# Kernel tuning notes

Hardware: AMD Instinct MI355X
Metric: run time of the kernel (lower is better)

Reference implementation:

```python
import jax, jax.numpy as jnp
import numpy as np

N, F, D, H = 8192, 128, 128, 2
LEAKY_ALPHA = 0.3  # keras.layers.LeakyReLU default


def setup_inputs() -> dict:
    key = jax.random.key(0)
    ks = jax.random.split(key, 8)
    x = jax.random.normal(ks[0], (N, F), dtype=jnp.float32)
    # sparse-ish binary adjacency with self loops, stored dense (as the module does)
    adj = (jax.random.uniform(ks[1], (N, N)) < 0.01).astype(jnp.float32)
    adj = jnp.clip(adj + jnp.eye(N, dtype=jnp.float32), 0.0, 1.0)
    s = 1.0 / np.sqrt(F)
    Wmap = jax.random.normal(ks[2], (H, F, D), dtype=jnp.float32) * s
    a1_w = jax.random.normal(ks[3], (H, D), dtype=jnp.float32) * (1.0 / np.sqrt(D))
    a2_w = jax.random.normal(ks[4], (H, D), dtype=jnp.float32) * (1.0 / np.sqrt(D))
    a1_b = jnp.zeros((H,), dtype=jnp.float32)
    a2_b = jnp.zeros((H,), dtype=jnp.float32)
    kernel = jax.random.normal(ks[5], (H, F, D), dtype=jnp.float32) * s
    bias = jnp.zeros((H, N, D), dtype=jnp.float32)
    return {"x": x, "adj": adj, "Wmap": Wmap, "a1_w": a1_w, "a1_b": a1_b,
            "a2_w": a2_w, "a2_b": a2_b, "kernel": kernel, "bias": bias}


def reference(x, adj, Wmap, a1_w, a1_b, a2_w, a2_b, kernel, bias):
    # per-head Conv1D(k=1, no bias): node-wise linear map  [H, N, D]
    mapped = jnp.einsum('nf,hfd->hnd', x, Wmap)
    # per-head Conv1D(k=1) scalar scores  [H, N]
    sa1 = jnp.einsum('hnd,hd->hn', mapped, a1_w) + a1_b[:, None]
    sa2 = jnp.einsum('hnd,hd->hn', mapped, a2_w) + a2_b[:, None]
    # additive score masked multiplicatively by adjacency:  [H, N, N]
    w = adj[None, :, :] * sa1[:, :, None] + adj[None, :, :] * sa2[:, None, :]
    w = jnp.where(w >= 0, w, LEAKY_ALPHA * w)
    att = jax.nn.softmax(w, axis=-1)  # softmax over neighbors (incl. zeroed entries, as in source)
    value = jnp.einsum('nf,hfd->hnd', x, kernel)
    out = jnp.einsum('hnm,hmd->hnd', att, value) + bias  # [H, N, D]
    return out.mean(axis=0)  # attn_heads_reduction='average', linear activation
```

## Files before the change

kernel.cpp:

```cpp
#include <hip/hip_runtime.h>

#define NN 8192
#define FF 128
#define DD 128
#define HH 2
#define ALPHA 0.3f
#define MAXNNZ 1024

typedef float v4f __attribute__((ext_vector_type(4)));

__global__ __launch_bounds__(256) void prep_kernel(
    const float* __restrict__ Wmap, const float* __restrict__ a1w,
    const float* __restrict__ a2w, const float* __restrict__ x,
    float* __restrict__ c1, float* __restrict__ c2, float* __restrict__ xsum) {
  int b = blockIdx.x;
  int t = threadIdx.x;
  if (b == 128) {
    int h = t >> 7, f = t & 127;
    const float* wrow = Wmap + ((size_t)h * FF + f) * DD;
    const float* a1 = a1w + h * DD;
    const float* a2 = a2w + h * DD;
    float s1 = 0.f, s2 = 0.f;
    #pragma unroll 8
    for (int d = 0; d < DD; d++) {
      float w = wrow[d];
      s1 += w * a1[d];
      s2 += w * a2[d];
    }
    c1[t] = s1;
    c2[t] = s2;
  } else {
    int f = t & 127, rh = t >> 7;
    const float* xp = x + ((size_t)(b * 64 + rh) * FF) + f;
    float s = 0.f;
    #pragma unroll 8
    for (int r = 0; r < 64; r += 2) s += xp[(size_t)r * FF];
    atomicAdd(&xsum[f], s);
  }
}

__global__ __launch_bounds__(128) void sa_kernel(
    const float* __restrict__ x, const float* __restrict__ c1,
    const float* __restrict__ c2, const float* __restrict__ a1b,
    const float* __restrict__ a2b, float* __restrict__ sa1, float* __restrict__ sa2p) {
  int n = blockIdx.x;
  int f = threadIdx.x;
  float xv = x[(size_t)n * FF + f];
  float p00 = xv * c1[f];
  float p01 = xv * c1[FF + f];
  float p10 = xv * c2[f];
  float p11 = xv * c2[FF + f];
  #pragma unroll
  for (int o = 32; o > 0; o >>= 1) {
    p00 += __shfl_down(p00, o);
    p01 += __shfl_down(p01, o);
    p10 += __shfl_down(p10, o);
    p11 += __shfl_down(p11, o);
  }
  __shared__ float part[2][4];
  int w = f >> 6;
  if ((f & 63) == 0) {
    part[w][0] = p00; part[w][1] = p01; part[w][2] = p10; part[w][3] = p11;
  }
  __syncthreads();
  if (f == 0) {
    sa1[n]      = part[0][0] + part[1][0] + a1b[0];
    sa1[NN + n] = part[0][1] + part[1][1] + a1b[1];
    ((float2*)sa2p)[n] = make_float2(part[0][2] + part[1][2] + a2b[0],
                                     part[0][3] + part[1][3] + a2b[1]);
  }
}

__global__ __launch_bounds__(256) void adj_scan(
    const float* __restrict__ adj, int* __restrict__ counts,
    int* __restrict__ idxw) {
  int i = blockIdx.x;
  __shared__ int idxbuf[MAXNNZ];
  __shared__ int cnt;
  int t = threadIdx.x;
  if (t == 0) cnt = 0;
  __syncthreads();
  const v4f* arow = (const v4f*)(adj + (size_t)i * NN);
  #pragma unroll
  for (int q = 0; q < 8; q++) {
    int f4 = q * 256 + t;
    v4f a = __builtin_nontemporal_load(&arow[f4]);
    int j0 = f4 * 4;
    if (a.x != 0.f) { int p = atomicAdd(&cnt, 1); if (p < MAXNNZ) idxbuf[p] = j0; }
    if (a.y != 0.f) { int p = atomicAdd(&cnt, 1); if (p < MAXNNZ) idxbuf[p] = j0 + 1; }
    if (a.z != 0.f) { int p = atomicAdd(&cnt, 1); if (p < MAXNNZ) idxbuf[p] = j0 + 2; }
    if (a.w != 0.f) { int p = atomicAdd(&cnt, 1); if (p < MAXNNZ) idxbuf[p] = j0 + 3; }
  }
  __syncthreads();
  int count = min(cnt, MAXNNZ);
  if (t == 0) counts[i] = count;
  int* dst = idxw + (size_t)i * MAXNNZ;
  for (int k = t; k < count; k += 256) dst[k] = idxbuf[k];
}

__global__ __launch_bounds__(256) void edge_gather(
    const int* __restrict__ counts, const int* __restrict__ idxw,
    const float* __restrict__ x, const float* __restrict__ sa1,
    const float* __restrict__ sa2p, const float* __restrict__ xsum,
    float* __restrict__ gs) {
  int i = blockIdx.x;
  __shared__ int idxbuf[MAXNNZ];
  __shared__ float em1buf[HH][MAXNNZ];
  __shared__ float wred[4][HH];
  __shared__ float sume_sh[HH];
  __shared__ v4f vred[HH][8][32];
  int t = threadIdx.x;
  int count = counts[i];
  const int* src = idxw + (size_t)i * MAXNNZ;
  for (int k = t; k < count; k += 256) idxbuf[k] = src[k];
  __syncthreads();

  float s10 = sa1[i];
  float s11 = sa1[NN + i];
  float l0 = 0.f, l1 = 0.f;
  for (int k = t; k < count; k += 256) {
    int j = idxbuf[k];
    float2 s2 = ((const float2*)sa2p)[j];
    float w0 = s10 + s2.x;
    float w1 = s11 + s2.y;
    w0 = (w0 >= 0.f) ? w0 : ALPHA * w0;
    w1 = (w1 >= 0.f) ? w1 : ALPHA * w1;
    float e0 = __expf(w0) - 1.f;
    float e1 = __expf(w1) - 1.f;
    em1buf[0][k] = e0;
    em1buf[1][k] = e1;
    l0 += e0;
    l1 += e1;
  }
  #pragma unroll
  for (int o = 32; o > 0; o >>= 1) {
    l0 += __shfl_down(l0, o);
    l1 += __shfl_down(l1, o);
  }
  int wid = t >> 6;
  if ((t & 63) == 0) { wred[wid][0] = l0; wred[wid][1] = l1; }
  __syncthreads();
  if (t == 0) {
    sume_sh[0] = wred[0][0] + wred[1][0] + wred[2][0] + wred[3][0];
    sume_sh[1] = wred[0][1] + wred[1][1] + wred[2][1] + wred[3][1];
  }
  __syncthreads();

  int sub = t & 31;
  int eg  = t >> 5;
  v4f acc0 = {0.f, 0.f, 0.f, 0.f}, acc1 = {0.f, 0.f, 0.f, 0.f};
  const v4f* xb = (const v4f*)x;
  #pragma unroll 4
  for (int k = eg; k < count; k += 8) {
    int j = idxbuf[k];
    v4f xv = xb[(size_t)j * 32 + sub];
    acc0 += em1buf[0][k] * xv;
    acc1 += em1buf[1][k] * xv;
  }
  vred[0][eg][sub] = acc0;
  vred[1][eg][sub] = acc1;
  __syncthreads();
  if (t < 64) {
    int h = t >> 5, s = t & 31;
    v4f v = vred[h][0][s];
    #pragma unroll
    for (int e = 1; e < 8; e++) v += vred[h][e][s];
    float inv = 0.5f / ((float)NN + sume_sh[h]);
    v4f xs = ((const v4f*)xsum)[s];
    v4f g = (v + xs) * inv;
    ((v4f*)(gs + (size_t)i * (HH * FF)))[h * 32 + s] = g;
  }
}

__global__ __launch_bounds__(256) void out_gemm(
    const float* __restrict__ gs, const float* __restrict__ kern,
    const float* __restrict__ bias, float* __restrict__ out) {
  int row0 = blockIdx.x * 32;
  __shared__ float Bl[64 * 128];
  __shared__ float Al[32 * 132];
  const float4* Bg4 = (const float4*)kern;
  const float4* Ag4 = (const float4*)(gs + (size_t)row0 * 256);
  float4* Bl4 = (float4*)Bl;
  int tid = threadIdx.x;
  int cg = tid & 31;
  int rg = tid >> 5;
  v4f acc[4];
  #pragma unroll
  for (int m = 0; m < 4; m++) acc[m] = (v4f){0.f, 0.f, 0.f, 0.f};

  for (int ka = 0; ka < 2; ka++) {
    __syncthreads();
    #pragma unroll
    for (int q = 0; q < 4; q++) {
      int idx = q * 256 + tid;
      int r = idx >> 5, c4 = idx & 31;
      float4 g = Ag4[r * 64 + ka * 32 + c4];
      *(float4*)&Al[r * 132 + c4 * 4] = g;
    }
    #pragma unroll
    for (int kpi = 0; kpi < 2; kpi++) {
      int kp = ka * 2 + kpi;
      __syncthreads();
      #pragma unroll
      for (int q = 0; q < 8; q++)
        Bl4[q * 256 + tid] = Bg4[kp * 2048 + q * 256 + tid];
      __syncthreads();
      #pragma unroll 4
      for (int kg = 0; kg < 16; kg++) {
        v4f bv0 = *(const v4f*)&Bl[(kg * 4 + 0) * 128 + cg * 4];
        v4f bv1 = *(const v4f*)&Bl[(kg * 4 + 1) * 128 + cg * 4];
        v4f bv2 = *(const v4f*)&Bl[(kg * 4 + 2) * 128 + cg * 4];
        v4f bv3 = *(const v4f*)&Bl[(kg * 4 + 3) * 128 + cg * 4];
        #pragma unroll
        for (int m = 0; m < 4; m++) {
          v4f a4 = *(const v4f*)&Al[(rg + m * 8) * 132 + kpi * 64 + kg * 4];
          acc[m] += a4.x * bv0;
          acc[m] += a4.y * bv1;
          acc[m] += a4.z * bv2;
          acc[m] += a4.w * bv3;
        }
      }
    }
  }

  #pragma unroll
  for (int m = 0; m < 4; m++) {
    int r = row0 + rg + m * 8;
    v4f b0 = *(const v4f*)&bias[((size_t)0 * NN + r) * DD + cg * 4];
    v4f b1 = *(const v4f*)&bias[((size_t)1 * NN + r) * DD + cg * 4];
    v4f o = acc[m] + 0.5f * (b0 + b1);
    *(v4f*)&out[(size_t)r * DD + cg * 4] = o;
  }
}

extern "C" void kernel_launch(void* const* d_in, const int* in_sizes, int n_in,
                              void* d_out, int out_size, void* d_ws, size_t ws_size,
                              hipStream_t stream) {
  const float* x    = (const float*)d_in[0];
  const float* adj  = (const float*)d_in[1];
  const float* Wmap = (const float*)d_in[2];
  const float* a1w  = (const float*)d_in[3];
  const float* a1b  = (const float*)d_in[4];
  const float* a2w  = (const float*)d_in[5];
  const float* a2b  = (const float*)d_in[6];
  const float* kern = (const float*)d_in[7];
  const float* bias = (const float*)d_in[8];
  float* out = (float*)d_out;
  float* ws  = (float*)d_ws;

  float* c1   = ws;
  float* c2   = ws + 256;
  float* sa1  = ws + 512;
  float* sa2p = ws + 16896;
  float* xsum = ws + 33280;
  float* gs   = ws + 33408;
  int*   counts = (int*)(ws + 2130560);
  int*   idxw   = (int*)(ws + 2138752);

  hipMemsetAsync(xsum, 0, FF * sizeof(float), stream);
  prep_kernel<<<129, 256, 0, stream>>>(Wmap, a1w, a2w, x, c1, c2, xsum);
  sa_kernel<<<NN, 128, 0, stream>>>(x, c1, c2, a1b, a2b, sa1, sa2p);
  adj_scan<<<NN, 256, 0, stream>>>(adj, counts, idxw);
  edge_gather<<<NN, 256, 0, stream>>>(counts, idxw, x, sa1, sa2p, xsum, gs);
  out_gemm<<<NN / 32, 256, 0, stream>>>(gs, kern, bias, out);
}
```

Before: 418.5 us.

## Fuse adjacency scan with edge gather and compute exp inline

Merges the adjacency row scan and the edge gather/aggregation into one kernel, so neighbor indices stay in shared memory instead of going through global memory and a second launch. The exponent weights are now computed inside the gather loop by each 32-lane group rather than in a separate pass staged through shared memory. Partial exp sums are reduced per group. This removes a kernel launch, the global index round-trip and a synchronisation phase. In exchange, each gather lane recomputes the exp redundantly, and scan and gather can no longer overlap across separate kernels.

```diff
diff --git a/kernel.cpp b/kernel.cpp
--- a/kernel.cpp
+++ b/kernel.cpp
@@ -71,15 +71,19 @@
   }
 }
 
-__global__ __launch_bounds__(256) void adj_scan(
-    const float* __restrict__ adj, int* __restrict__ counts,
-    int* __restrict__ idxw) {
+__global__ __launch_bounds__(256) void gat_fused(
+    const float* __restrict__ adj, const float* __restrict__ x,
+    const float* __restrict__ sa1, const float* __restrict__ sa2p,
+    const float* __restrict__ xsum, float* __restrict__ gs) {
   int i = blockIdx.x;
   __shared__ int idxbuf[MAXNNZ];
   __shared__ int cnt;
+  __shared__ float esum_sh[8][HH];
+  __shared__ v4f vred[HH][8][32];
   int t = threadIdx.x;
   if (t == 0) cnt = 0;
   __syncthreads();
+
   const v4f* arow = (const v4f*)(adj + (size_t)i * NN);
   #pragma unroll
   for (int q = 0; q < 8; q++) {
@@ -93,82 +97,47 @@
   }
   __syncthreads();
   int count = min(cnt, MAXNNZ);
-  if (t == 0) counts[i] = count;
-  int* dst = idxw + (size_t)i * MAXNNZ;
-  for (int k = t; k < count; k += 256) dst[k] = idxbuf[k];
-}
-
-__global__ __launch_bounds__(256) void edge_gather(
-    const int* __restrict__ counts, const int* __restrict__ idxw,
-    const float* __restrict__ x, const float* __restrict__ sa1,
-    const float* __restrict__ sa2p, const float* __restrict__ xsum,
-    float* __restrict__ gs) {
-  int i = blockIdx.x;
-  __shared__ int idxbuf[MAXNNZ];
-  __shared__ float em1buf[HH][MAXNNZ];
-  __shared__ float wred[4][HH];
-  __shared__ float sume_sh[HH];
-  __shared__ v4f vred[HH][8][32];
-  int t = threadIdx.x;
-  int count = counts[i];
-  const int* src = idxw + (size_t)i * MAXNNZ;
-  for (int k = t; k < count; k += 256) idxbuf[k] = src[k];
-  __syncthreads();
 
   float s10 = sa1[i];
   float s11 = sa1[NN + i];
-  float l0 = 0.f, l1 = 0.f;
-  for (int k = t; k < count; k += 256) {
+  int sub = t & 31;
+  int eg  = t >> 5;
+  v4f acc0 = {0.f, 0.f, 0.f, 0.f}, acc1 = {0.f, 0.f, 0.f, 0.f};
+  float le0 = 0.f, le1 = 0.f;
+  const v4f* xb = (const v4f*)x;
+  const float2* s2p = (const float2*)sa2p;
+  #pragma unroll 2
+  for (int k = eg; k < count; k += 8) {
     int j = idxbuf[k];
-    float2 s2 = ((const float2*)sa2p)[j];
+    float2 s2 = s2p[j];
+    v4f xv = xb[(size_t)j * 32 + sub];
     float w0 = s10 + s2.x;
     float w1 = s11 + s2.y;
     w0 = (w0 >= 0.f) ? w0 : ALPHA * w0;
     w1 = (w1 >= 0.f) ? w1 : ALPHA * w1;
     float e0 = __expf(w0) - 1.f;
     float e1 = __expf(w1) - 1.f;
-    em1buf[0][k] = e0;
-    em1buf[1][k] = e1;
-    l0 += e0;
-    l1 += e1;
-  }
-  #pragma unroll
-  for (int o = 32; o > 0; o >>= 1) {
-    l0 += __shfl_down(l0, o);
-    l1 += __shfl_down(l1, o);
-  }
-  int wid = t >> 6;
-  if ((t & 63) == 0) { wred[wid][0] = l0; wred[wid][1] = l1; }
-  __syncthreads();
-  if (t == 0) {
-    sume_sh[0] = wred[0][0] + wred[1][0] + wred[2][0] + wred[3][0];
-    sume_sh[1] = wred[0][1] + wred[1][1] + wred[2][1] + wred[3][1];
-  }
-  __syncthreads();
-
-  int sub = t & 31;
-  int eg  = t >> 5;
-  v4f acc0 = {0.f, 0.f, 0.f, 0.f}, acc1 = {0.f, 0.f, 0.f, 0.f};
-  const v4f* xb = (const v4f*)x;
-  #pragma unroll 4
-  for (int k = eg; k < count; k += 8) {
-    int j = idxbuf[k];
-    v4f xv = xb[(size_t)j * 32 + sub];
-    acc0 += em1buf[0][k] * xv;
-    acc1 += em1buf[1][k] * xv;
+    acc0 += e0 * xv;
+    acc1 += e1 * xv;
+    le0 += e0;
+    le1 += e1;
   }
   vred[0][eg][sub] = acc0;
   vred[1][eg][sub] = acc1;
-  __syncthreads();
+  if (sub == 0) { esum_sh[eg][0] = le0; esum_sh[eg][1] = le1; }
+  __syncthreads();
+
   if (t < 64) {
     int h = t >> 5, s = t & 31;
     v4f v = vred[h][0][s];
     #pragma unroll
     for (int e = 1; e < 8; e++) v += vred[h][e][s];
-    float inv = 0.5f / ((float)NN + sume_sh[h]);
+    float sume = 0.f;
+    #pragma unroll
+    for (int e = 0; e < 8; e++) sume += esum_sh[e][h];
+    float inv = 0.5f / ((float)NN + sume);
     v4f xs = ((const v4f*)xsum)[s];
-    v4f g = (v + xs) * inv;
-    ((v4f*)(gs + (size_t)i * (HH * FF)))[h * 32 + s] = g;
+    ((v4f*)(gs + (size_t)i * (HH * FF)))[h * 32 + s] = (v + xs) * inv;
   }
 }
 
@@ -254,13 +223,10 @@
   float* sa2p = ws + 16896;
   float* xsum = ws + 33280;
   float* gs   = ws + 33408;
-  int*   counts = (int*)(ws + 2130560);
-  int*   idxw   = (int*)(ws + 2138752);
 
   hipMemsetAsync(xsum, 0, FF * sizeof(float), stream);
   prep_kernel<<<129, 256, 0, stream>>>(Wmap, a1w, a2w, x, c1, c2, xsum);
   sa_kernel<<<NN, 128, 0, stream>>>(x, c1, c2, a1b, a2b, sa1, sa2p);
-  adj_scan<<<NN, 256, 0, stream>>>(adj, counts, idxw);
-  edge_gather<<<NN, 256, 0, stream>>>(counts, idxw, x, sa1, sa2p, xsum, gs);
+  gat_fused<<<NN, 256, 0, stream>>>(adj, x, sa1, sa2p, xsum, gs);
   out_gemm<<<NN / 32, 256, 0, stream>>>(gs, kern, bias, out);
 }
```

Result: no change. 414.2 us (-1.0%).
